# Optimization experiments

Hardware: AMD Instinct MI355X
Metric: run time of the kernel (lower is better)

The kernel has to match this reference:

```python
import jax, jax.numpy as jnp
import numpy as np

N_HEAD = 16
N_EMBD = 1024
HEAD_DIM = N_EMBD // N_HEAD  # 64
ROPE_BASE = 10000.0


def _rotary_cos_sin(T, dim, dtype=jnp.float32):
    # matches Rotary: inv_freq over even indices, cos/sin cached in bfloat16
    inv_freq = 1.0 / (ROPE_BASE ** (jnp.arange(0, dim, 2, dtype=jnp.float32) / dim))
    freqs = jnp.arange(T, dtype=jnp.float32)[:, None] * inv_freq[None, :]  # [T, dim/2]
    cos = jnp.cos(freqs).astype(jnp.bfloat16).astype(dtype)
    sin = jnp.sin(freqs).astype(jnp.bfloat16).astype(dtype)
    # shape [1, T, 1, dim/2] to broadcast over (B, T, H, d)
    return cos[None, :, None, :], sin[None, :, None, :]


def _apply_rotary(x, cos, sin):
    d = x.shape[3] // 2
    x1, x2 = x[..., :d], x[..., d:]
    y1 = x1 * cos + x2 * sin
    y2 = -x1 * sin + x2 * cos
    return jnp.concatenate([y1, y2], axis=3).astype(x.dtype)


def setup_inputs() -> dict:
    key = jax.random.key(0)
    ks = jax.random.split(key, 8)
    B, T, C = 2, 2048, N_EMBD
    scale = C ** -0.5  # realistic linear-layer init scale
    x = jax.random.normal(ks[0], (B, T, C), dtype=jnp.float32)
    Wq1 = jax.random.normal(ks[1], (C, C), dtype=jnp.float32) * scale
    Wk1 = jax.random.normal(ks[2], (C, C), dtype=jnp.float32) * scale
    Wq2 = jax.random.normal(ks[3], (C, C), dtype=jnp.float32) * scale
    Wk2 = jax.random.normal(ks[4], (C, C), dtype=jnp.float32) * scale
    Wv = jax.random.normal(ks[5], (C, C), dtype=jnp.float32) * scale
    Wout = jax.random.normal(ks[6], (C, C), dtype=jnp.float32) * scale
    return {"x": x, "Wq1": Wq1, "Wk1": Wk1, "Wq2": Wq2, "Wk2": Wk2, "Wv": Wv, "Wout": Wout}


def reference(x, Wq1, Wk1, Wq2, Wk2, Wv, Wout):
    B, T, C = x.shape
    H, D = N_HEAD, HEAD_DIM

    def proj(W):
        # torch nn.Linear(bias=False): y = x @ W.T
        return (x @ W.T).reshape(B, T, H, D)

    q1, k1 = proj(Wq1), proj(Wk1)
    q2, k2 = proj(Wq2), proj(Wk2)
    v = proj(Wv)

    cos, sin = _rotary_cos_sin(T, D, x.dtype)
    q1, k1 = _apply_rotary(q1, cos, sin), _apply_rotary(k1, cos, sin)
    q2, k2 = _apply_rotary(q2, cos, sin), _apply_rotary(k2, cos, sin)

    # two bilinear score maps, elementwise product, causal mask
    s1 = jnp.einsum('bqhd,bkhd->bhqk', q1, k1)  # [B,H,T,T]
    s2 = jnp.einsum('bqhd,bkhd->bhqk', q2, k2)
    causal = jnp.tril(jnp.ones((T, T), dtype=bool))
    pattern = jnp.where(causal[None, None], (s1 / D) * (s2 / D), 0.0)

    y = jnp.einsum('bhqk,bkhd->bqhd', pattern, v).reshape(B, T, C)
    return y @ Wout.T
```

## Files before the change

kernel.cpp:

```cpp
#include <hip/hip_runtime.h>
#include <hip/hip_bf16.h>
#include <math.h>

typedef __bf16 bf16;
typedef __bf16 bf16x8 __attribute__((ext_vector_type(8)));
typedef float  f32x4  __attribute__((ext_vector_type(4)));

#define NB    2
#define NT    2048
#define NH    16
#define ND    64
#define NC    1024
#define NBT   4096
#define NQT   32

#define AS1C(p) ((const __attribute__((address_space(1))) void*)(p))
#define AS3(p)  ((__attribute__((address_space(3))) void*)(p))

#define MFMA(a,b,c) __builtin_amdgcn_mfma_f32_16x16x32_bf16(a, b, c, 0, 0, 0)

struct WPtrs { const float* p[6]; };

__global__ void prep_kernel(const float* __restrict__ x, WPtrs w,
                            bf16* __restrict__ Xbf, bf16* __restrict__ Wcat,
                            float2* __restrict__ tbl)
{
    const int bid = blockIdx.x;
    if (bid < 4096) {
        const int i = (bid * 256 + threadIdx.x) * 4;
        float4 v = *reinterpret_cast<const float4*>(x + i);
        Xbf[i+0] = (bf16)v.x; Xbf[i+1] = (bf16)v.y;
        Xbf[i+2] = (bf16)v.z; Xbf[i+3] = (bf16)v.w;
    } else if (bid < 10240) {
        const int r   = bid - 4096;
        const int mat = r >> 10;
        const int off = ((r & 1023) * 256 + threadIdx.x) * 4;
        float4 v = *reinterpret_cast<const float4*>(w.p[mat] + off);
        bf16* d = Wcat + (size_t)mat * NC * NC + off;
        d[0] = (bf16)v.x; d[1] = (bf16)v.y; d[2] = (bf16)v.z; d[3] = (bf16)v.w;
    } else {
        const int i = (bid - 10240) * 256 + threadIdx.x;
        const int t = i >> 5, j = i & 31;
        float invf = 1.0f / powf(10000.0f, (float)j * (1.0f/32.0f));
        float fr = (float)t * invf;
        float2 cs;
        cs.x = (float)(bf16)cosf(fr);
        cs.y = (float)(bf16)sinf(fr);
        tbl[i] = cs;
    }
}

__global__ __launch_bounds__(256, 2)
void gemm_proj(const bf16* __restrict__ A, const bf16* __restrict__ Bw,
               bf16* __restrict__ qkv, const float2* __restrict__ tbl)
{
    __shared__ bf16 smem[4*8192];

    const int tid  = threadIdx.x;
    const int lane = tid & 63;
    const int w    = tid >> 6;
    const int wr   = w >> 1;
    const int wc   = w & 1;

    const int id  = blockIdx.x;
    const int swz = (id & 7) * 160 + (id >> 3);
    const int by  = swz / 40, bx = swz % 40;
    const int row0 = by * 128, col0 = bx * 128;

    const int lo  = lane & 15;
    const int hi  = lane >> 4;

    const int hrow = w*16 + (lane >> 2);
    const int hcol = ((lane & 3) ^ ((lane >> 3) & 3)) * 8;

    f32x4 acc[4][4] = {};

    auto stageHalf = [&](int s) {
        char* base = (char*)smem + (s & 3) * 16384;
        const int k0 = s * 32;
        #pragma unroll
        for (int i = 0; i < 2; ++i) {
            __builtin_amdgcn_global_load_lds(
                AS1C(A + (size_t)(row0 + i*64 + hrow) * NC + k0 + hcol),
                AS3(base + i*4096 + w*1024), 16, 0, 0);
            __builtin_amdgcn_global_load_lds(
                AS1C(Bw + (size_t)(col0 + i*64 + hrow) * NC + k0 + hcol),
                AS3(base + 8192 + i*4096 + w*1024), 16, 0, 0);
        }
    };

    stageHalf(0);
    stageHalf(1);

    const int csw = (lo >> 1) & 3;
    for (int s = 0; s < 32; ++s) {
        if (s < 31) asm volatile("s_waitcnt vmcnt(4)" ::: "memory");
        else        asm volatile("s_waitcnt vmcnt(0)" ::: "memory");
        __builtin_amdgcn_s_barrier();
        asm volatile("" ::: "memory");
        if (s + 2 < 32) stageHalf(s + 2);

        const char* As = (const char*)smem + (s & 3) * 16384;
        const char* Bs = As + 8192;

        bf16x8 af[4], bfr[4];
        #pragma unroll
        for (int m = 0; m < 4; ++m) {
            const int ar = wr*64 + m*16 + lo;
            af[m] = *reinterpret_cast<const bf16x8*>(As + ar*64 + ((hi ^ csw) * 16));
        }
        #pragma unroll
        for (int n = 0; n < 4; ++n) {
            const int br = wc*64 + n*16 + lo;
            bfr[n] = *reinterpret_cast<const bf16x8*>(Bs + br*64 + ((hi ^ csw) * 16));
        }
        __builtin_amdgcn_s_setprio(1);
        #pragma unroll
        for (int m = 0; m < 4; ++m)
            #pragma unroll
            for (int n = 0; n < 4; ++n)
                acc[m][n] = MFMA(af[m], bfr[n], acc[m][n]);
        __builtin_amdgcn_s_setprio(0);
    }
    __syncthreads();

    bf16* Ct = smem;
    const int p  = col0 >> 10;
    const int h0 = (col0 >> 6) & (NH-1);
    const int rb = hi * 4;

    if (p < 4) {
        const float qsc = (p == 0 || p == 2) ? 0.015625f : 1.0f;
        #pragma unroll
        for (int m = 0; m < 4; ++m)
            #pragma unroll
            for (int r = 0; r < 4; ++r) {
                const int rl = wr*64 + m*16 + rb + r;
                const int t  = (row0 + rl) & (NT-1);
                const unsigned key = ((unsigned)(rl >> 2) & 3) << 5;
                #pragma unroll
                for (int n = 0; n < 2; ++n) {
                    const int j = n*16 + lo;
                    float2 cs = tbl[t*32 + j];
                    float a1 = acc[m][n][r];
                    float a2 = acc[m][n+2][r];
                    const int c1 = wc*64 + j;
                    const int c2 = c1 + 32;
                    *(bf16*)((char*)Ct + (unsigned)(rl*256 + (((unsigned)c1*2) ^ key)))
                        = (bf16)((a1*cs.x + a2*cs.y) * qsc);
                    *(bf16*)((char*)Ct + (unsigned)(rl*256 + (((unsigned)c2*2) ^ key)))
                        = (bf16)((a2*cs.x - a1*cs.y) * qsc);
                }
            }
        __syncthreads();
        #pragma unroll
        for (int it = 0; it < 8; ++it) {
            const int chunk = it*256 + tid;
            const int rl = chunk >> 4;
            const int cc = chunk & 15;
            const unsigned key = ((unsigned)(rl >> 2) & 3) << 5;
            bf16x8 val = *reinterpret_cast<const bf16x8*>(
                (const char*)Ct + ((unsigned)rl*256 + (((unsigned)cc*16) ^ key)));
            const int rowg = row0 + rl;
            const int b = rowg >> 11;
            const int t = rowg & (NT-1);
            const int hh = h0 + (cc >> 3);
            const int d  = (cc & 7) * 8;
            *reinterpret_cast<bf16x8*>(
                qkv + ((((size_t)p*NB + b)*NH + hh)*NT + t)*ND + d) = val;
        }
    } else {
        #pragma unroll
        for (int m = 0; m < 4; ++m)
            #pragma unroll
            for (int r = 0; r < 4; ++r) {
                const int rl = wr*64 + m*16 + rb + r;
                #pragma unroll
                for (int n = 0; n < 4; ++n) {
                    const int c = wc*64 + n*16 + lo;
                    *(bf16*)((char*)Ct + (unsigned)(c*256 + (((unsigned)rl*2) ^ ((c&7)<<4))))
                        = (bf16)acc[m][n][r];
                }
            }
        __syncthreads();
        const int b  = row0 >> 11;
        const int t0 = row0 & (NT-1);
        #pragma unroll
        for (int it = 0; it < 8; ++it) {
            const int chunk = it*256 + tid;
            const int c   = chunk >> 4;
            const int tcc = chunk & 15;
            bf16x8 val = *reinterpret_cast<const bf16x8*>(
                (const char*)Ct + (unsigned)(c*256 + (((unsigned)tcc*16) ^ ((c&7)<<4))));
            const int hh = h0 + (c >> 6);
            const int d  = c & 63;
            *reinterpret_cast<bf16x8*>(
                qkv + (((size_t)4*NB + b)*NH + hh)*(size_t)NT*ND
                    + (size_t)d*NT + t0 + tcc*8) = val;
        }
    }
}

__global__ __launch_bounds__(256)
void gemm_out(const bf16* __restrict__ A, const bf16* __restrict__ Bw,
              float* __restrict__ Cp)
{
    __shared__ bf16 smem[4*6144];

    const int tid  = threadIdx.x;
    const int lane = tid & 63;
    const int w    = tid >> 6;
    const int wr   = w >> 1;
    const int wc   = w & 1;
    const int row0 = blockIdx.y * 128;
    const int col0 = blockIdx.x * 64;

    const int lo  = lane & 15;
    const int hi  = lane >> 4;

    const int hrow = w*16 + (lane >> 2);
    const int hcol = ((lane & 3) ^ ((lane >> 3) & 3)) * 8;

    f32x4 acc[4][2] = {};

    auto stageHalf = [&](int s) {
        char* base = (char*)smem + (s & 3) * 12288;
        const int k0 = s * 32;
        #pragma unroll
        for (int i = 0; i < 2; ++i)
            __builtin_amdgcn_global_load_lds(
                AS1C(A + (size_t)(row0 + i*64 + hrow) * NC + k0 + hcol),
                AS3(base + i*4096 + w*1024), 16, 0, 0);
        __builtin_amdgcn_global_load_lds(
            AS1C(Bw + (size_t)(col0 + hrow) * NC + k0 + hcol),
            AS3(base + 8192 + w*1024), 16, 0, 0);
    };

    stageHalf(0);
    stageHalf(1);

    const int csw = (lo >> 1) & 3;
    for (int s = 0; s < 32; ++s) {
        if (s < 31) asm volatile("s_waitcnt vmcnt(3)" ::: "memory");
        else        asm volatile("s_waitcnt vmcnt(0)" ::: "memory");
        __builtin_amdgcn_s_barrier();
        asm volatile("" ::: "memory");
        if (s + 2 < 32) stageHalf(s + 2);

        const char* As = (const char*)smem + (s & 3) * 12288;
        const char* Bs = As + 8192;

        bf16x8 af[4], bfr[2];
        #pragma unroll
        for (int m = 0; m < 4; ++m) {
            const int ar = wr*64 + m*16 + lo;
            af[m] = *reinterpret_cast<const bf16x8*>(As + ar*64 + ((hi ^ csw) * 16));
        }
        #pragma unroll
        for (int n = 0; n < 2; ++n) {
            const int br = wc*32 + n*16 + lo;
            bfr[n] = *reinterpret_cast<const bf16x8*>(Bs + br*64 + ((hi ^ csw) * 16));
        }
        __builtin_amdgcn_s_setprio(1);
        #pragma unroll
        for (int m = 0; m < 4; ++m)
            #pragma unroll
            for (int n = 0; n < 2; ++n)
                acc[m][n] = MFMA(af[m], bfr[n], acc[m][n]);
        __builtin_amdgcn_s_setprio(0);
    }

    const int rb = hi * 4;
    #pragma unroll
    for (int m = 0; m < 4; ++m)
        #pragma unroll
        for (int n = 0; n < 2; ++n)
            #pragma unroll
            for (int r = 0; r < 4; ++r) {
                int row = row0 + wr*64 + m*16 + rb + r;
                int col = col0 + wc*32 + n*16 + lo;
                Cp[(size_t)row * NC + col] = acc[m][n][r];
            }
}

__global__ __launch_bounds__(256, 2)
void attn_kernel(const bf16* __restrict__ qkv, bf16* __restrict__ Y)
{
    __shared__ bf16 K1s[3*4096];
    __shared__ bf16 K2s[3*4096];
    __shared__ bf16 Vts[3*4096];
    __shared__ bf16 Pl [4][1024];

    const int tid  = threadIdx.x;
    const int lane = tid & 63;
    const int w    = tid >> 6;

    const int lin  = blockIdx.x;
    const int xcd  = lin & 7;
    const int slot = lin >> 3;
    const int pair = xcd * 4 + (slot >> 4);
    const int qa   = slot & 15;
    const int h    = pair >> 1;
    const int b    = pair & 1;
    const int qb   = NQT - 1 - qa;

    const size_t plane = (size_t)NB * NH * NT * ND;
    const size_t bh    = ((size_t)b * NH + h) * (size_t)NT * ND;
    const bf16* Q1 = qkv + 0*plane + bh;
    const bf16* K1 = qkv + 1*plane + bh;
    const bf16* Q2 = qkv + 2*plane + bh;
    const bf16* K2 = qkv + 3*plane + bh;
    const bf16* V  = qkv + 4*plane + bh;

    const int lo  = lane & 15;
    const int hi  = lane >> 4;
    const int hi8 = hi * 8;

    bf16x8 q1fa[2], q2fa[2], q1fb[2], q2fb[2];
    #pragma unroll
    for (int dd = 0; dd < 2; ++dd) {
        const size_t ra  = (size_t)(qa*64 + w*16 + lo) * ND + dd*32 + hi8;
        const size_t rbq = (size_t)(qb*64 + w*16 + lo) * ND + dd*32 + hi8;
        q1fa[dd] = *reinterpret_cast<const bf16x8*>(Q1 + ra);
        q2fa[dd] = *reinterpret_cast<const bf16x8*>(Q2 + ra);
        q1fb[dd] = *reinterpret_cast<const bf16x8*>(Q1 + rbq);
        q2fb[dd] = *reinterpret_cast<const bf16x8*>(Q2 + rbq);
    }

    f32x4 yacca[4] = {}, yaccb[4] = {};

    const int srow = tid >> 3;
    const int ssw  = ((tid & 7) ^ (srow & 7)) * 8;

    auto stageK = [&](int buf, int k0) {
        #pragma unroll
        for (int i = 0; i < 2; ++i) {
            const unsigned loff = (unsigned)(buf*8192 + i*4096 + w*1024);
            __builtin_amdgcn_global_load_lds(
                AS1C(K1 + (size_t)(k0 + i*32 + srow) * ND + ssw),
                AS3((char*)K1s + loff), 16, 0, 0);
            __builtin_amdgcn_global_load_lds(
                AS1C(K2 + (size_t)(k0 + i*32 + srow) * ND + ssw),
                AS3((char*)K2s + loff), 16, 0, 0);
        }
    };
    auto stageVT = [&](int buf, int k0) {
        #pragma unroll
        for (int i = 0; i < 2; ++i) {
            const int inst = w*2 + i;
            const int d    = inst*8 + (lane >> 3);
            const int sc   = ((lane & 7) ^ ((lane >> 3) & 7)) * 8;
            __builtin_amdgcn_global_load_lds(
                AS1C(V + (size_t)d * NT + k0 + sc),
                AS3((char*)Vts + (unsigned)(buf*8192 + inst*1024)), 16, 0, 0);
        }
    };

    stageK(0, 0);  stageVT(0, 0);
    stageK(1, 64); stageVT(1, 64);

    int cur = 0;
    for (int kt = 0; kt <= qb; ++kt) {
        if (kt < qb) asm volatile("s_waitcnt vmcnt(6)" ::: "memory");
        else         asm volatile("s_waitcnt vmcnt(0)" ::: "memory");
        __syncthreads();
        if (kt + 2 <= qb) {
            int nx = cur + 2; if (nx >= 3) nx -= 3;
            stageK(nx, (kt + 2) * 64);
            stageVT(nx, (kt + 2) * 64);
        }

        const bool doA = (kt <= qa);
        const bf16* K1b = K1s + cur*4096;
        const bf16* K2b = K2s + cur*4096;
        const char* Vb  = (const char*)Vts + cur*8192;

        f32x4 s1a[4] = {}, s2a[4] = {}, s1b[4] = {}, s2b[4] = {};
        __builtin_amdgcn_s_setprio(1);
        #pragma unroll
        for (int dd = 0; dd < 2; ++dd)
            #pragma unroll
            for (int sub = 0; sub < 4; ++sub) {
                const unsigned kb = (unsigned)((sub*16 + lo)*128 + (((dd*4 + hi) ^ (lo & 7)) * 16));
                bf16x8 k1f = *reinterpret_cast<const bf16x8*>((const char*)K1b + kb);
                bf16x8 k2f = *reinterpret_cast<const bf16x8*>((const char*)K2b + kb);
                s1b[sub] = MFMA(q1fb[dd], k1f, s1b[sub]);
                s2b[sub] = MFMA(q2fb[dd], k2f, s2b[sub]);
                if (doA) {
                    s1a[sub] = MFMA(q1fa[dd], k1f, s1a[sub]);
                    s2a[sub] = MFMA(q2fa[dd], k2f, s2a[sub]);
                }
            }
        __builtin_amdgcn_s_setprio(0);

        #define COMBINE(S1, S2, DIAG)                                                  \
            _Pragma("unroll")                                                          \
            for (int sub = 0; sub < 4; ++sub)                                          \
                _Pragma("unroll")                                                      \
                for (int r = 0; r < 4; ++r) {                                          \
                    const int row = hi*4 + r;                                          \
                    const int col = sub*16 + lo;                                       \
                    const unsigned byte = (unsigned)(row*128 + (((col>>3) ^ (row&7))*16) + (col&7)*2); \
                    float pv = S1[sub][r] * S2[sub][r];                                \
                    if (DIAG && col > w*16 + row) pv = 0.0f;                           \
                    *(bf16*)((char*)Pl[w] + byte) = (bf16)pv;                          \
                }

        if (kt == qb) { COMBINE(s1b, s2b, true) } else { COMBINE(s1b, s2b, false) }
        asm volatile("s_waitcnt lgkmcnt(0)" ::: "memory");
        __builtin_amdgcn_sched_barrier(0);

        bf16x8 vfr[2][4];
        __builtin_amdgcn_s_setprio(1);
        #pragma unroll
        for (int ks = 0; ks < 2; ++ks) {
            const unsigned pby = (unsigned)(lo*128 + (((ks*4 + hi) ^ (lo & 7)) * 16));
            bf16x8 pfb = *reinterpret_cast<const bf16x8*>((const char*)Pl[w] + pby);
            #pragma unroll
            for (int n = 0; n < 4; ++n) {
                const unsigned vby = (unsigned)((n*16 + lo)*128 + (((ks*4 + hi) ^ (lo & 7)) * 16));
                vfr[ks][n] = *reinterpret_cast<const bf16x8*>(Vb + vby);
                yaccb[n] = MFMA(pfb, vfr[ks][n], yaccb[n]);
            }
        }
        __builtin_amdgcn_s_setprio(0);

        if (doA) {
            asm volatile("s_waitcnt lgkmcnt(0)" ::: "memory");
            __builtin_amdgcn_sched_barrier(0);
            if (kt == qa) { COMBINE(s1a, s2a, true) } else { COMBINE(s1a, s2a, false) }
            asm volatile("s_waitcnt lgkmcnt(0)" ::: "memory");
            __builtin_amdgcn_sched_barrier(0);
            __builtin_amdgcn_s_setprio(1);
            #pragma unroll
            for (int ks = 0; ks < 2; ++ks) {
                const unsigned pby = (unsigned)(lo*128 + (((ks*4 + hi) ^ (lo & 7)) * 16));
                bf16x8 pfa = *reinterpret_cast<const bf16x8*>((const char*)Pl[w] + pby);
                #pragma unroll
                for (int n = 0; n < 4; ++n)
                    yacca[n] = MFMA(pfa, vfr[ks][n], yacca[n]);
            }
            __builtin_amdgcn_s_setprio(0);
        }
        #undef COMBINE

        cur += 1; if (cur >= 3) cur -= 3;
    }

    auto writeOut = [&](int q0, const f32x4* ya) {
        #pragma unroll
        for (int n = 0; n < 4; ++n)
            #pragma unroll
            for (int r = 0; r < 4; ++r) {
                const int row = hi*4 + r;
                const int col = n*16 + lo;
                const unsigned byte = (unsigned)(row*128 + (((col>>3) ^ (row&7))*16) + (col&7)*2);
                *(bf16*)((char*)Pl[w] + byte) = (bf16)ya[n][r];
            }
        asm volatile("s_waitcnt lgkmcnt(0)" ::: "memory");
        __builtin_amdgcn_sched_barrier(0);
        #pragma unroll
        for (int pass = 0; pass < 2; ++pass) {
            const int idx = pass*64 + lane;
            const int row = idx >> 3;
            const int cc  = idx & 7;
            bf16x8 val = *reinterpret_cast<const bf16x8*>(
                (const char*)Pl[w] + row*128 + ((cc ^ (row&7))*16));
            const int t = q0 + w*16 + row;
            const int c = h*ND + cc*8;
            *reinterpret_cast<bf16x8*>(Y + ((size_t)b*NT + t)*NC + c) = val;
        }
    };
    writeOut(qa*64, yacca);
    writeOut(qb*64, yaccb);
}

extern "C" void kernel_launch(void* const* d_in, const int* in_sizes, int n_in,
                              void* d_out, int out_size, void* d_ws, size_t ws_size,
                              hipStream_t stream)
{
    const float* x = (const float*)d_in[0];

    char* ws = (char*)d_ws;
    bf16*   Xbf   = (bf16*)ws;
    bf16*   Wcat  = (bf16*)(ws + (size_t)NBT*NC*2);
    bf16*   QKV   = (bf16*)(ws + (size_t)NBT*NC*2 + (size_t)6*NC*NC*2);
    bf16*   Ybf   = (bf16*)((char*)QKV + (size_t)5*NBT*NC*2);
    float2* tbl   = (float2*)((char*)Ybf + (size_t)NBT*NC*2);
    bf16*   Woutb = Wcat + (size_t)5*NC*NC;

    WPtrs wp;
    wp.p[0] = (const float*)d_in[1]; wp.p[1] = (const float*)d_in[2];
    wp.p[2] = (const float*)d_in[3]; wp.p[3] = (const float*)d_in[4];
    wp.p[4] = (const float*)d_in[5]; wp.p[5] = (const float*)d_in[6];

    prep_kernel<<<dim3(10496), 256, 0, stream>>>(x, wp, Xbf, Wcat, tbl);

    gemm_proj<<<dim3(1280), 256, 0, stream>>>(Xbf, Wcat, QKV, tbl);
    attn_kernel<<<dim3(512), 256, 0, stream>>>(QKV, Ybf);
    gemm_out<<<dim3(NC/64, NBT/128), 256, 0, stream>>>(Ybf, Woutb, (float*)d_out);
}
```

Baseline: 146.2 us.

## Triple-buffer projection GEMM for three blocks per CU and remap tiles per XCD

```diff
diff --git a/kernel.cpp b/kernel.cpp
--- a/kernel.cpp
+++ b/kernel.cpp
@@ -50,11 +50,11 @@
     }
 }
 
-__global__ __launch_bounds__(256, 2)
+__global__ __launch_bounds__(256, 3)
 void gemm_proj(const bf16* __restrict__ A, const bf16* __restrict__ Bw,
                bf16* __restrict__ qkv, const float2* __restrict__ tbl)
 {
-    __shared__ bf16 smem[4*8192];
+    __shared__ bf16 smem[3*8192];
 
     const int tid  = threadIdx.x;
     const int lane = tid & 63;
@@ -63,8 +63,10 @@
     const int wc   = w & 1;
 
     const int id  = blockIdx.x;
-    const int swz = (id & 7) * 160 + (id >> 3);
-    const int by  = swz / 40, bx = swz % 40;
+    const int xcd = id & 7;
+    const int r   = id >> 3;
+    const int bx  = r >> 2;
+    const int by  = xcd * 4 + (r & 3);
     const int row0 = by * 128, col0 = bx * 128;
 
     const int lo  = lane & 15;
@@ -75,8 +77,8 @@
 
     f32x4 acc[4][4] = {};
 
-    auto stageHalf = [&](int s) {
-        char* base = (char*)smem + (s & 3) * 16384;
+    auto stageHalf = [&](int s, int slot) {
+        char* base = (char*)smem + slot * 16384;
         const int k0 = s * 32;
         #pragma unroll
         for (int i = 0; i < 2; ++i) {
@@ -89,18 +91,22 @@
         }
     };
 
-    stageHalf(0);
-    stageHalf(1);
+    stageHalf(0, 0);
+    stageHalf(1, 1);
 
     const int csw = (lo >> 1) & 3;
+    int slot = 0;
     for (int s = 0; s < 32; ++s) {
         if (s < 31) asm volatile("s_waitcnt vmcnt(4)" ::: "memory");
         else        asm volatile("s_waitcnt vmcnt(0)" ::: "memory");
         __builtin_amdgcn_s_barrier();
         asm volatile("" ::: "memory");
-        if (s + 2 < 32) stageHalf(s + 2);
-
-        const char* As = (const char*)smem + (s & 3) * 16384;
+        if (s + 2 < 32) {
+            int nx = slot + 2; if (nx >= 3) nx -= 3;
+            stageHalf(s + 2, nx);
+        }
+
+        const char* As = (const char*)smem + slot * 16384;
         const char* Bs = As + 8192;
 
         bf16x8 af[4], bfr[4];
@@ -121,6 +127,8 @@
             for (int n = 0; n < 4; ++n)
                 acc[m][n] = MFMA(af[m], bfr[n], acc[m][n]);
         __builtin_amdgcn_s_setprio(0);
+
+        slot += 1; if (slot >= 3) slot -= 3;
     }
     __syncthreads();
 
@@ -134,16 +142,16 @@
         #pragma unroll
         for (int m = 0; m < 4; ++m)
             #pragma unroll
-            for (int r = 0; r < 4; ++r) {
-                const int rl = wr*64 + m*16 + rb + r;
+            for (int r2 = 0; r2 < 4; ++r2) {
+                const int rl = wr*64 + m*16 + rb + r2;
                 const int t  = (row0 + rl) & (NT-1);
                 const unsigned key = ((unsigned)(rl >> 2) & 3) << 5;
                 #pragma unroll
                 for (int n = 0; n < 2; ++n) {
                     const int j = n*16 + lo;
                     float2 cs = tbl[t*32 + j];
-                    float a1 = acc[m][n][r];
-                    float a2 = acc[m][n+2][r];
+                    float a1 = acc[m][n][r2];
+                    float a2 = acc[m][n+2][r2];
                     const int c1 = wc*64 + j;
                     const int c2 = c1 + 32;
                     *(bf16*)((char*)Ct + (unsigned)(rl*256 + (((unsigned)c1*2) ^ key)))
@@ -173,13 +181,13 @@
         #pragma unroll
         for (int m = 0; m < 4; ++m)
             #pragma unroll
-            for (int r = 0; r < 4; ++r) {
-                const int rl = wr*64 + m*16 + rb + r;
+            for (int r2 = 0; r2 < 4; ++r2) {
+                const int rl = wr*64 + m*16 + rb + r2;
                 #pragma unroll
                 for (int n = 0; n < 4; ++n) {
                     const int c = wc*64 + n*16 + lo;
                     *(bf16*)((char*)Ct + (unsigned)(c*256 + (((unsigned)rl*2) ^ ((c&7)<<4))))
-                        = (bf16)acc[m][n][r];
+                        = (bf16)acc[m][n][r2];
                 }
             }
         __syncthreads();
```

Measured after the change: 137.7 us. 5.8% less time.
